# Kernel tuning notes

Hardware: AMD Instinct MI355X
Metric: run time of the kernel (lower is better)

## Reference

```python
import jax, jax.numpy as jnp
import numpy as np

B, T, C = 2, 4096, 768
H = 12
D = C // H  # head_dim = 64


def setup_inputs() -> dict:
    key = jax.random.key(0)
    kx, kq, kk, kv, ko = jax.random.split(key, 5)
    s = 1.0 / np.sqrt(C)  # keep activations well-scaled
    return {
        "x": jax.random.normal(kx, (B, T, C), dtype=jnp.float32),
        "wq": jax.random.normal(kq, (C, C), dtype=jnp.float32) * s,
        "wk": jax.random.normal(kk, (C, C), dtype=jnp.float32) * s,
        "wv": jax.random.normal(kv, (C, C), dtype=jnp.float32) * s,
        "wo": jax.random.normal(ko, (C, C), dtype=jnp.float32) * s,
    }


def reference(x, wq, wk, wv, wo):
    b, t, c = x.shape
    # projections (torch Linear: y = x @ W.T); split heads -> (B,H,T,D)
    q = (x @ wq.T).reshape(b, t, H, D).transpose(0, 2, 1, 3)
    k = (x @ wk.T).reshape(b, t, H, D).transpose(0, 2, 1, 3)
    v = (x @ wv.T).reshape(b, t, H, D).transpose(0, 2, 1, 3)
    scale = 1.0 / jnp.sqrt(jnp.asarray(D, dtype=x.dtype))
    scores = jnp.einsum("bhqd,bhkd->bhqk", q, k) * scale  # (B,H,T,T)
    causal = jnp.tril(jnp.ones((t, t), dtype=bool))
    scores = jnp.where(causal, scores, jnp.asarray(-jnp.inf, dtype=scores.dtype))
    attn = jax.nn.softmax(scores, axis=-1)
    ctx = jnp.einsum("bhqk,bhkd->bhqd", attn, v)  # (B,H,T,D)
    ctx = ctx.transpose(0, 2, 1, 3).reshape(b, t, c)
    return ctx @ wo.T
```

## Files before the change

### kernel.cpp

```cpp
#include <hip/hip_runtime.h>
#include <hip/hip_bf16.h>

#define B_  2
#define T_  4096
#define C_  768
#define H_  12
#define D_  64
#define MTOT (B_*T_)

typedef __bf16 bf16;
typedef __bf16 bf16x8 __attribute__((ext_vector_type(8)));
typedef __bf16 bf16x4 __attribute__((ext_vector_type(4)));
typedef float  f32x4  __attribute__((ext_vector_type(4)));
typedef unsigned int u32x4 __attribute__((ext_vector_type(4)));

__device__ __forceinline__ void gl_lds16(const bf16* g, bf16* l) {
    __builtin_amdgcn_global_load_lds(
        (const __attribute__((address_space(1))) void*)g,
        (__attribute__((address_space(3))) void*)l, 16, 0, 0);
}

__device__ __forceinline__ void pswap32_16(unsigned int& x, unsigned int& y) {
    auto r1 = __builtin_amdgcn_permlane32_swap(x, y, false, false);
    auto r2 = __builtin_amdgcn_permlane16_swap(r1[0], r1[1], false, false);
    x = r2[0]; y = r2[1];
}
__device__ __forceinline__ unsigned int cvtpk(float lo, float hi) {
    unsigned int r;
    asm("v_cvt_pk_bf16_f32 %0, %1, %2" : "=v"(r) : "v"(lo), "v"(hi));
    return r;
}

__global__ __launch_bounds__(256) void cvt_bf16(const float* __restrict__ src,
                                                bf16* __restrict__ dst, int n8) {
    int i = blockIdx.x * 256 + threadIdx.x;
    if (i >= n8) return;
    const float4* s4 = (const float4*)src;
    float4 a = s4[2*(size_t)i], b = s4[2*(size_t)i+1];
    bf16x8 o;
    o[0]=(bf16)a.x; o[1]=(bf16)a.y; o[2]=(bf16)a.z; o[3]=(bf16)a.w;
    o[4]=(bf16)b.x; o[5]=(bf16)b.y; o[6]=(bf16)b.z; o[7]=(bf16)b.w;
    *(bf16x8*)(dst + 8*(size_t)i) = o;
}

__global__ __launch_bounds__(256) void cvt_bf16_w4(const float* __restrict__ w0,
                                                   const float* __restrict__ w1,
                                                   const float* __restrict__ w2,
                                                   const float* __restrict__ w3,
                                                   bf16* __restrict__ d0,
                                                   bf16* __restrict__ d1,
                                                   bf16* __restrict__ d2,
                                                   bf16* __restrict__ d3) {
    int z = blockIdx.y;
    const float* src = (z==0)?w0:(z==1)?w1:(z==2)?w2:w3;
    bf16* dst = (z==0)?d0:(z==1)?d1:(z==2)?d2:d3;
    int i = blockIdx.x * 256 + threadIdx.x;
    const float4* s4 = (const float4*)src;
    float4 a = s4[2*(size_t)i], b = s4[2*(size_t)i+1];
    bf16x8 o;
    o[0]=(bf16)a.x; o[1]=(bf16)a.y; o[2]=(bf16)a.z; o[3]=(bf16)a.w;
    o[4]=(bf16)b.x; o[5]=(bf16)b.y; o[6]=(bf16)b.z; o[7]=(bf16)b.w;
    *(bf16x8*)(dst + 8*(size_t)i) = o;
}

__global__ __launch_bounds__(256) void gemm_qkv(const bf16* __restrict__ xb,
                                                const bf16* __restrict__ wqb,
                                                const bf16* __restrict__ wkb,
                                                const bf16* __restrict__ wvb,
                                                bf16* __restrict__ qo,
                                                bf16* __restrict__ ko,
                                                bf16* __restrict__ vto) {
    int z = blockIdx.z;
    const bf16* w = (z == 0) ? wqb : (z == 1) ? wkb : wvb;
    bf16* dst = (z == 0) ? qo : (z == 1) ? ko : vto;
    int mbase = blockIdx.x * 128;
    int nbase = blockIdx.y * 128;
    __shared__ bf16 As[2][128][32];
    __shared__ bf16 Bs[2][128][32];
    int tid  = threadIdx.x;
    int wave = tid >> 6, lane = tid & 63;
    int wm = (wave >> 1) * 64, wn = (wave & 1) * 64;
    int lr = lane & 15, lg = lane >> 4;
    int srow0 = tid >> 2, scol0 = tid & 3;
    int srow1 = (tid + 256) >> 2, scol1 = (tid + 256) & 3;
    const bf16* xa0 = xb + (size_t)(mbase + srow0) * C_ + scol0 * 8;
    const bf16* xa1 = xb + (size_t)(mbase + srow1) * C_ + scol1 * 8;
    const bf16* wa0 = w  + (size_t)(nbase + srow0) * C_ + scol0 * 8;
    const bf16* wa1 = w  + (size_t)(nbase + srow1) * C_ + scol1 * 8;
#define GSTAGE(kb_, cb_) do { \
        gl_lds16(xa0 + (kb_), &As[cb_][srow0][scol0 * 8]); \
        gl_lds16(xa1 + (kb_), &As[cb_][srow1][scol1 * 8]); \
        gl_lds16(wa0 + (kb_), &Bs[cb_][srow0][scol0 * 8]); \
        gl_lds16(wa1 + (kb_), &Bs[cb_][srow1][scol1 * 8]); \
    } while (0)
    f32x4 acc[4][4] = {};
    GSTAGE(0, 0);
    __syncthreads();
    int cur = 0;
    for (int kb = 0; kb < C_; kb += 32) {
        if (kb + 32 < C_) GSTAGE(kb + 32, cur ^ 1);
        bf16x8 af[4], bfr[4];
        #pragma unroll
        for (int mt = 0; mt < 4; ++mt) af[mt]  = *(const bf16x8*)(&As[cur][wm + mt*16 + lr][lg*8]);
        #pragma unroll
        for (int nt = 0; nt < 4; ++nt) bfr[nt] = *(const bf16x8*)(&Bs[cur][wn + nt*16 + lr][lg*8]);
        #pragma unroll
        for (int mt = 0; mt < 4; ++mt)
            #pragma unroll
            for (int nt = 0; nt < 4; ++nt)
                acc[mt][nt] = __builtin_amdgcn_mfma_f32_16x16x32_bf16(af[mt], bfr[nt], acc[mt][nt], 0, 0, 0);
        __syncthreads();
        cur ^= 1;
    }
#undef GSTAGE
    float sc = (z == 0) ? 0.18033688011112042f : 1.0f;
    int m0 = mbase + wm + (lg << 2);
    int n0 = nbase + wn + lr;
    if (z < 2) {
        #pragma unroll
        for (int mt = 0; mt < 4; ++mt) {
            #pragma unroll
            for (int nt = 0; nt < 4; ++nt) {
                int n = n0 + nt * 16;
                int h = n >> 6, d = n & 63;
                #pragma unroll
                for (int r = 0; r < 4; ++r) {
                    int m = m0 + mt * 16 + r;
                    int b = m >> 12, t = m & 4095;
                    dst[(((size_t)b * H_ + h) * T_ + t) * 64 + d] = (bf16)(acc[mt][nt][r] * sc);
                }
            }
        }
    } else {
        #pragma unroll
        for (int mt = 0; mt < 4; ++mt) {
            int m = m0 + mt * 16;
            int b = m >> 12, t = m & 4095;
            #pragma unroll
            for (int nt = 0; nt < 4; ++nt) {
                int n = n0 + nt * 16;
                int h = n >> 6, d = n & 63;
                bf16x4 pk;
                #pragma unroll
                for (int r = 0; r < 4; ++r) pk[r] = (bf16)acc[mt][nt][r];
                *(bf16x4*)(dst + (((size_t)b * H_ + h) * 64 + d) * T_ + t) = pk;
            }
        }
    }
}

__global__ __launch_bounds__(256) void gemm_out(const bf16* __restrict__ ctx,
                                                const bf16* __restrict__ wob,
                                                float* __restrict__ out) {
    int mbase = blockIdx.x * 128;
    int nbase = blockIdx.y * 128;
    __shared__ bf16 As[2][128][32];
    __shared__ bf16 Bs[2][128][32];
    int tid  = threadIdx.x;
    int wave = tid >> 6, lane = tid & 63;
    int wm = (wave >> 1) * 64, wn = (wave & 1) * 64;
    int lr = lane & 15, lg = lane >> 4;
    int srow0 = tid >> 2, scol0 = tid & 3;
    int srow1 = (tid + 256) >> 2, scol1 = (tid + 256) & 3;
    const bf16* xa0 = ctx + (size_t)(mbase + srow0) * C_ + scol0 * 8;
    const bf16* xa1 = ctx + (size_t)(mbase + srow1) * C_ + scol1 * 8;
    const bf16* wa0 = wob + (size_t)(nbase + srow0) * C_ + scol0 * 8;
    const bf16* wa1 = wob + (size_t)(nbase + srow1) * C_ + scol1 * 8;
#define GSTAGE(kb_, cb_) do { \
        gl_lds16(xa0 + (kb_), &As[cb_][srow0][scol0 * 8]); \
        gl_lds16(xa1 + (kb_), &As[cb_][srow1][scol1 * 8]); \
        gl_lds16(wa0 + (kb_), &Bs[cb_][srow0][scol0 * 8]); \
        gl_lds16(wa1 + (kb_), &Bs[cb_][srow1][scol1 * 8]); \
    } while (0)
    f32x4 acc[4][4] = {};
    GSTAGE(0, 0);
    __syncthreads();
    int cur = 0;
    for (int kb = 0; kb < C_; kb += 32) {
        if (kb + 32 < C_) GSTAGE(kb + 32, cur ^ 1);
        bf16x8 af[4], bfr[4];
        #pragma unroll
        for (int mt = 0; mt < 4; ++mt) af[mt]  = *(const bf16x8*)(&As[cur][wm + mt*16 + lr][lg*8]);
        #pragma unroll
        for (int nt = 0; nt < 4; ++nt) bfr[nt] = *(const bf16x8*)(&Bs[cur][wn + nt*16 + lr][lg*8]);
        #pragma unroll
        for (int mt = 0; mt < 4; ++mt)
            #pragma unroll
            for (int nt = 0; nt < 4; ++nt)
                acc[mt][nt] = __builtin_amdgcn_mfma_f32_16x16x32_bf16(af[mt], bfr[nt], acc[mt][nt], 0, 0, 0);
        __syncthreads();
        cur ^= 1;
    }
#undef GSTAGE
    int m0 = mbase + wm + (lg << 2);
    int n0 = nbase + wn + lr;
    #pragma unroll
    for (int mt = 0; mt < 4; ++mt)
        #pragma unroll
        for (int nt = 0; nt < 4; ++nt)
            #pragma unroll
            for (int r = 0; r < 4; ++r)
                out[(size_t)(m0 + mt * 16 + r) * C_ + n0 + nt * 16] = acc[mt][nt][r];
}

__device__ __forceinline__ void attn_store(const f32x4 (&o)[4], float l, bf16* __restrict__ ctx,
                                           int b, int qrow, int h, int lg) {
    float inv = 1.0f / l;
    #pragma unroll
    for (int dt = 0; dt < 4; ++dt) {
        bf16x4 pk;
        #pragma unroll
        for (int r = 0; r < 4; ++r) pk[r] = (bf16)(o[dt][r] * inv);
        *(bf16x4*)(ctx + ((size_t)b * T_ + qrow) * C_ + h * 64 + dt * 16 + lg * 4) = pk;
    }
}

__global__ __launch_bounds__(256) void attn(const bf16* __restrict__ q,
                                            const bf16* __restrict__ k,
                                            const bf16* __restrict__ vt,
                                            bf16* __restrict__ ctx) {
    int idx = blockIdx.x;
    int qt = 63 - idx / 24;
    int bh = idx % 24;
    int b = bh / H_, h = bh % H_;
    int tid = threadIdx.x;
    int wave = tid >> 6, lane = tid & 63;
    int lr = lane & 15, lg = lane >> 4;

    __shared__ bf16 Ks[2][64][64];
    __shared__ bf16 Vs[2][64][64];

    const bf16* qp = q  + (size_t)bh * T_ * 64;
    const bf16* kp = k  + (size_t)bh * T_ * 64;
    const bf16* vp = vt + (size_t)bh * 64 * (size_t)T_;

    int r0 = tid >> 3, c0 = tid & 7;
    int cs = (c0 ^ (r0 & 7)) * 8;
    const bf16* kstg = kp + (size_t)r0 * 64 + cs;
    const bf16* vstg = vp + (size_t)r0 * T_ + cs;

#define STAGE(kb_, cb_) do { \
        const bf16* ks_ = kstg + (size_t)(kb_) * 64 * 64; \
        const bf16* vs_ = vstg + (size_t)(kb_) * 64; \
        gl_lds16(ks_,                   &Ks[cb_][r0][c0 * 8]); \
        gl_lds16(ks_ + 32 * 64,         &Ks[cb_][32 + r0][c0 * 8]); \
        gl_lds16(vs_,                   &Vs[cb_][r0][c0 * 8]); \
        gl_lds16(vs_ + (size_t)32 * T_, &Vs[cb_][32 + r0][c0 * 8]); \
    } while (0)

    const float NEGINF = -__builtin_inff();

    int qb = qt * 64 + wave * 16;
    int n  = qt + 1;
    int qrow = qb + lr;

    int sw = lr & 7;
    int col0 = (lg ^ sw) * 8;
    int col1 = ((4 | lg) ^ sw) * 8;

    bf16x8 qf[2];
    #pragma unroll
    for (int c = 0; c < 2; ++c)
        qf[c] = *(const bf16x8*)(qp + (size_t)(qb + lr) * 64 + c * 32 + lg * 8);

    f32x4 o[4] = {};
    float lsum = 0.f;
    const f32x4 fz = {};

    STAGE(0, 0);
    __syncthreads();
    int cur = 0;

    for (int kb = 0; kb < n; ++kb) {
        int kv = kb * 64;
        if (kb + 1 < n) STAGE(kb + 1, cur ^ 1);

        f32x4 s[4];
        __builtin_amdgcn_s_setprio(1);
        #pragma unroll
        for (int nt = 0; nt < 4; ++nt) {
            bf16x8 kf0 = *(const bf16x8*)(&Ks[cur][nt * 16 + lr][col0]);
            s[nt] = __builtin_amdgcn_mfma_f32_16x16x32_bf16(kf0, qf[0], fz, 0, 0, 0);
        }
        #pragma unroll
        for (int nt = 0; nt < 4; ++nt) {
            bf16x8 kf1 = *(const bf16x8*)(&Ks[cur][nt * 16 + lr][col1]);
            s[nt] = __builtin_amdgcn_mfma_f32_16x16x32_bf16(kf1, qf[1], s[nt], 0, 0, 0);
        }
        __builtin_amdgcn_s_setprio(0);
        if (kb == qt) {
            #pragma unroll
            for (int nt = 0; nt < 4; ++nt)
                #pragma unroll
                for (int r = 0; r < 4; ++r) {
                    int key = kv + nt * 16 + lg * 4 + r;
                    s[nt][r] = (key > qrow) ? NEGINF : s[nt][r];
                }
        }
        #pragma unroll
        for (int nt = 0; nt < 4; ++nt) {
            #pragma unroll
            for (int r = 0; r < 4; ++r)
                s[nt][r] = __builtin_amdgcn_exp2f(s[nt][r]);
            lsum += (s[nt][0] + s[nt][1]) + (s[nt][2] + s[nt][3]);
        }
        unsigned int dpk[8];
        #pragma unroll
        for (int nt = 0; nt < 4; ++nt) {
            dpk[2*nt]   = cvtpk(s[nt][0], s[nt][1]);
            dpk[2*nt+1] = cvtpk(s[nt][2], s[nt][3]);
        }
        unsigned int pw[2][4];
        #pragma unroll
        for (int c2 = 0; c2 < 2; ++c2)
            #pragma unroll
            for (int pr = 0; pr < 2; ++pr) {
                unsigned int x = dpk[4*c2 + pr], y = dpk[4*c2 + 2 + pr];
                pswap32_16(x, y);
                pw[c2][pr] = x;
                pw[c2][2+pr] = y;
            }
        __builtin_amdgcn_s_setprio(1);
        #pragma unroll
        for (int c2 = 0; c2 < 2; ++c2) {
            u32x4 pt;
            pt[0] = pw[c2][0]; pt[1] = pw[c2][1]; pt[2] = pw[c2][2]; pt[3] = pw[c2][3];
            bf16x8 pf = __builtin_bit_cast(bf16x8, pt);
            int vcol = c2 ? col1 : col0;
            #pragma unroll
            for (int dt = 0; dt < 4; ++dt) {
                bf16x8 vfr = *(const bf16x8*)(&Vs[cur][dt * 16 + lr][vcol]);
                o[dt] = __builtin_amdgcn_mfma_f32_16x16x32_bf16(vfr, pf, o[dt], 0, 0, 0);
            }
        }
        __builtin_amdgcn_s_setprio(0);

        __syncthreads();
        cur ^= 1;
    }
#undef STAGE

    float l = lsum;
    l += __shfl_xor(l, 16, 64);
    l += __shfl_xor(l, 32, 64);
    attn_store(o, l, ctx, b, qrow, h, lg);
}

extern "C" void kernel_launch(void* const* d_in, const int* in_sizes, int n_in,
                              void* d_out, int out_size, void* d_ws, size_t ws_size,
                              hipStream_t stream) {
    const float* x  = (const float*)d_in[0];
    const float* wq = (const float*)d_in[1];
    const float* wk = (const float*)d_in[2];
    const float* wv = (const float*)d_in[3];
    const float* wo = (const float*)d_in[4];
    float* out = (float*)d_out;

    char* ws = (char*)d_ws;
    const size_t SZ_XB = (size_t)MTOT * C_ * sizeof(bf16);
    const size_t SZ_W  = (size_t)C_ * C_ * sizeof(bf16);
    bf16* xb  = (bf16*)(ws);
    bf16* wqb = (bf16*)(ws + SZ_XB);
    bf16* wkb = (bf16*)(ws + SZ_XB + SZ_W);
    bf16* wvb = (bf16*)(ws + SZ_XB + 2 * SZ_W);
    bf16* wob = (bf16*)(ws + SZ_XB + 3 * SZ_W);
    bf16* qb  = (bf16*)(ws + SZ_XB + 4 * SZ_W);
    bf16* kb  = (bf16*)(ws + 2 * SZ_XB + 4 * SZ_W);
    bf16* vtb = (bf16*)(ws + 3 * SZ_XB + 4 * SZ_W);
    bf16* ctb = (bf16*)(ws + 4 * SZ_XB + 4 * SZ_W);

    cvt_bf16<<<3072, 256, 0, stream>>>(x, xb, MTOT * C_ / 8);
    cvt_bf16_w4<<<dim3(288, 4), 256, 0, stream>>>(wq, wk, wv, wo, wqb, wkb, wvb, wob);

    gemm_qkv<<<dim3(MTOT / 128, C_ / 128, 3), 256, 0, stream>>>(xb, wqb, wkb, wvb, qb, kb, vtb);
    attn<<<1536, 256, 0, stream>>>(qb, kb, vtb, ctb);
    gemm_out<<<dim3(MTOT / 128, C_ / 128), 256, 0, stream>>>(ctb, wob, out);
}
```

Measured before the change: 228.4 us.

## Triple-buffer GEMM LDS staging and vectorize Q/K epilogue stores via swapped MFMA operands

Both projection GEMMs move from double to triple buffering in LDS. Loads are issued two k-steps ahead, and a partial vmcnt wait plus a raw barrier replaces the full __syncthreads. For the Q and K outputs, the MFMA operands are swapped so each lane holds 4 consecutive d values, which lets the epilogue write bf16x4 vectors instead of scattered scalar bf16 stores. This raises LDS use per block and relies on hand-tuned waitcnt counts being correct.

Result: slower. 251.8 us (+10.3%).

```diff
diff --git a/kernel.cpp b/kernel.cpp
--- a/kernel.cpp
+++ b/kernel.cpp
@@ -75,8 +75,8 @@
     bf16* dst = (z == 0) ? qo : (z == 1) ? ko : vto;
     int mbase = blockIdx.x * 128;
     int nbase = blockIdx.y * 128;
-    __shared__ bf16 As[2][128][32];
-    __shared__ bf16 Bs[2][128][32];
+    __shared__ bf16 As[3][128][32];
+    __shared__ bf16 Bs[3][128][32];
     int tid  = threadIdx.x;
     int wave = tid >> 6, lane = tid & 63;
     int wm = (wave >> 1) * 64, wn = (wave & 1) * 64;
@@ -95,43 +95,62 @@
     } while (0)
     f32x4 acc[4][4] = {};
     GSTAGE(0, 0);
-    __syncthreads();
-    int cur = 0;
-    for (int kb = 0; kb < C_; kb += 32) {
-        if (kb + 32 < C_) GSTAGE(kb + 32, cur ^ 1);
+    GSTAGE(32, 1);
+    asm volatile("s_waitcnt vmcnt(4)" ::: "memory");
+    __builtin_amdgcn_s_barrier();
+    int cur = 0, stg = 2;
+    for (int t = 0; t < 24; ++t) {
+        if (t + 2 < 24) GSTAGE((t + 2) * 32, stg);
         bf16x8 af[4], bfr[4];
         #pragma unroll
         for (int mt = 0; mt < 4; ++mt) af[mt]  = *(const bf16x8*)(&As[cur][wm + mt*16 + lr][lg*8]);
         #pragma unroll
         for (int nt = 0; nt < 4; ++nt) bfr[nt] = *(const bf16x8*)(&Bs[cur][wn + nt*16 + lr][lg*8]);
-        #pragma unroll
-        for (int mt = 0; mt < 4; ++mt)
-            #pragma unroll
-            for (int nt = 0; nt < 4; ++nt)
-                acc[mt][nt] = __builtin_amdgcn_mfma_f32_16x16x32_bf16(af[mt], bfr[nt], acc[mt][nt], 0, 0, 0);
-        __syncthreads();
-        cur ^= 1;
+        if (z < 2) {
+            #pragma unroll
+            for (int mt = 0; mt < 4; ++mt)
+                #pragma unroll
+                for (int nt = 0; nt < 4; ++nt)
+                    acc[mt][nt] = __builtin_amdgcn_mfma_f32_16x16x32_bf16(bfr[nt], af[mt], acc[mt][nt], 0, 0, 0);
+        } else {
+            #pragma unroll
+            for (int mt = 0; mt < 4; ++mt)
+                #pragma unroll
+                for (int nt = 0; nt < 4; ++nt)
+                    acc[mt][nt] = __builtin_amdgcn_mfma_f32_16x16x32_bf16(af[mt], bfr[nt], acc[mt][nt], 0, 0, 0);
+        }
+        if (t + 2 < 24) {
+            asm volatile("s_waitcnt vmcnt(4)" ::: "memory");
+            __builtin_amdgcn_s_barrier();
+        } else if (t + 1 < 24) {
+            asm volatile("s_waitcnt vmcnt(0)" ::: "memory");
+            __builtin_amdgcn_s_barrier();
+        }
+        cur = (cur == 2) ? 0 : cur + 1;
+        stg = (stg == 2) ? 0 : stg + 1;
     }
 #undef GSTAGE
     float sc = (z == 0) ? 0.18033688011112042f : 1.0f;
-    int m0 = mbase + wm + (lg << 2);
-    int n0 = nbase + wn + lr;
     if (z < 2) {
+        int m0 = mbase + wm + lr;
+        int n0 = nbase + wn + (lg << 2);
         #pragma unroll
         for (int mt = 0; mt < 4; ++mt) {
+            int m = m0 + mt * 16;
+            int b = m >> 12, t = m & 4095;
             #pragma unroll
             for (int nt = 0; nt < 4; ++nt) {
                 int n = n0 + nt * 16;
                 int h = n >> 6, d = n & 63;
+                bf16x4 pk;
                 #pragma unroll
-                for (int r = 0; r < 4; ++r) {
-                    int m = m0 + mt * 16 + r;
-                    int b = m >> 12, t = m & 4095;
-                    dst[(((size_t)b * H_ + h) * T_ + t) * 64 + d] = (bf16)(acc[mt][nt][r] * sc);
-                }
+                for (int r = 0; r < 4; ++r) pk[r] = (bf16)(acc[mt][nt][r] * sc);
+                *(bf16x4*)(dst + (((size_t)b * H_ + h) * T_ + t) * 64 + d) = pk;
             }
         }
     } else {
+        int m0 = mbase + wm + (lg << 2);
+        int n0 = nbase + wn + lr;
         #pragma unroll
         for (int mt = 0; mt < 4; ++mt) {
             int m = m0 + mt * 16;
@@ -154,8 +173,8 @@
                                                 float* __restrict__ out) {
     int mbase = blockIdx.x * 128;
     int nbase = blockIdx.y * 128;
-    __shared__ bf16 As[2][128][32];
-    __shared__ bf16 Bs[2][128][32];
+    __shared__ bf16 As[3][128][32];
+    __shared__ bf16 Bs[3][128][32];
     int tid  = threadIdx.x;
     int wave = tid >> 6, lane = tid & 63;
     int wm = (wave >> 1) * 64, wn = (wave & 1) * 64;
@@ -174,10 +193,12 @@
     } while (0)
     f32x4 acc[4][4] = {};
     GSTAGE(0, 0);
-    __syncthreads();
-    int cur = 0;
-    for (int kb = 0; kb < C_; kb += 32) {
-        if (kb + 32 < C_) GSTAGE(kb + 32, cur ^ 1);
+    GSTAGE(32, 1);
+    asm volatile("s_waitcnt vmcnt(4)" ::: "memory");
+    __builtin_amdgcn_s_barrier();
+    int cur = 0, stg = 2;
+    for (int t = 0; t < 24; ++t) {
+        if (t + 2 < 24) GSTAGE((t + 2) * 32, stg);
         bf16x8 af[4], bfr[4];
         #pragma unroll
         for (int mt = 0; mt < 4; ++mt) af[mt]  = *(const bf16x8*)(&As[cur][wm + mt*16 + lr][lg*8]);
@@ -188,8 +209,15 @@
             #pragma unroll
             for (int nt = 0; nt < 4; ++nt)
                 acc[mt][nt] = __builtin_amdgcn_mfma_f32_16x16x32_bf16(af[mt], bfr[nt], acc[mt][nt], 0, 0, 0);
-        __syncthreads();
-        cur ^= 1;
+        if (t + 2 < 24) {
+            asm volatile("s_waitcnt vmcnt(4)" ::: "memory");
+            __builtin_amdgcn_s_barrier();
+        } else if (t + 1 < 24) {
+            asm volatile("s_waitcnt vmcnt(0)" ::: "memory");
+            __builtin_amdgcn_s_barrier();
+        }
+        cur = (cur == 2) ? 0 : cur + 1;
+        stg = (stg == 2) ? 0 : stg + 1;
     }
 #undef GSTAGE
     int m0 = mbase + wm + (lg << 2);
```
